# Kernel optimization log

Hardware: AMD Instinct MI355X
Metric: run time of the kernel (lower is better)

The kernel has to match this reference:

```python
import jax, jax.numpy as jnp
import numpy as np

N = 100000
EPS = 1e-5

def gcn_conv(x, W, b, src, dst, n):
    # linear transform first (PyG GCNConv): [N, H]
    h = x @ W
    # add self-loops
    loop = jnp.arange(n, dtype=src.dtype)
    s = jnp.concatenate([src, loop])
    d = jnp.concatenate([dst, loop])
    # symmetric normalization deg^{-1/2}[s] * deg^{-1/2}[d]
    deg = jax.ops.segment_sum(jnp.ones_like(d, dtype=h.dtype), d, num_segments=n)
    dinv = jnp.where(deg > 0, jax.lax.rsqrt(jnp.maximum(deg, 1.0) * 0 + jnp.where(deg > 0, deg, 1.0)), 0.0)
    norm = dinv[s] * dinv[d]
    msg = h[s] * norm[:, None]          # gather + scale: [E+N, H]
    out = jax.ops.segment_sum(msg, d, num_segments=n)  # scatter-add
    return out + b

def batch_norm(x, gamma, beta):
    mu = jnp.mean(x, axis=0)
    var = jnp.mean((x - mu) ** 2, axis=0)  # biased var, as BatchNorm1d training
    return (x - mu) * jax.lax.rsqrt(var + EPS) * gamma + beta

def setup_inputs() -> dict:
    key = jax.random.key(0)
    ks = jax.random.split(key, 8)
    D, H, O = 64, 64, 32
    E = 1600000
    x = jax.random.normal(ks[0], (N, D), dtype=jnp.float32)
    edge_index = jax.random.randint(ks[1], (2, E), 0, N, dtype=jnp.int64)
    W1 = jax.random.normal(ks[2], (D, H), dtype=jnp.float32) / np.sqrt(D)
    b1 = jnp.zeros((H,), dtype=jnp.float32)
    W2 = jax.random.normal(ks[3], (H, H), dtype=jnp.float32) / np.sqrt(H)
    b2 = jnp.zeros((H,), dtype=jnp.float32)
    gamma1 = jnp.ones((H,), dtype=jnp.float32); beta1 = jnp.zeros((H,), dtype=jnp.float32)
    gamma2 = jnp.ones((H,), dtype=jnp.float32); beta2 = jnp.zeros((H,), dtype=jnp.float32)
    Wfc = jax.random.normal(ks[4], (H, O), dtype=jnp.float32) / np.sqrt(H)
    bfc = jnp.zeros((O,), dtype=jnp.float32)
    return {"x": x, "edge_index": edge_index, "W1": W1, "b1": b1, "gamma1": gamma1, "beta1": beta1,
            "W2": W2, "b2": b2, "gamma2": gamma2, "beta2": beta2, "Wfc": Wfc, "bfc": bfc}

def reference(x, edge_index, W1, b1, gamma1, beta1, W2, b2, gamma2, beta2, Wfc, bfc):
    src, dst = edge_index[0], edge_index[1]
    h = jax.nn.relu(gcn_conv(x, W1, b1, src, dst, N))
    h = batch_norm(h, gamma1, beta1)
    h = jax.nn.relu(gcn_conv(h, W2, b2, src, dst, N))
    h = batch_norm(h, gamma2, beta2)
    return h @ Wfc + bfc
```

## Files before the change

kernel.cpp:

```cpp
#include <hip/hip_runtime.h>
#include <hip/hip_bf16.h>
#include <cstdint>
#include <cstddef>

#define NS 8
#define SCHUNK 12500
#define BKB 512
#define SUBC 32

static __device__ __forceinline__ unsigned pack_bf16(float a, float b) {
  __hip_bfloat16 lo = __float2bfloat16(a), hi = __float2bfloat16(b);
  unsigned short ulo = *reinterpret_cast<unsigned short*>(&lo);
  unsigned short uhi = *reinterpret_cast<unsigned short*>(&hi);
  return ((unsigned)uhi << 16) | ulo;
}
static __device__ __forceinline__ float blo(unsigned u) {
  union { unsigned q; float f; } x; x.q = u << 16; return x.f;
}
static __device__ __forceinline__ float bhi(unsigned u) {
  union { unsigned q; float f; } x; x.q = u & 0xffff0000u; return x.f;
}


__launch_bounds__(256)
__global__ void bucket_kernel(const int* __restrict__ src, const int* __restrict__ dst,
                              int E, int cap, unsigned magic,
                              int* __restrict__ bcur,
                              int* __restrict__ bkt_d, int* __restrict__ bkt_s) {
  __shared__ int cnt8[NS], base8[NS], gbase8[NS], cur8[NS];
  __shared__ int stg_d[3200], stg_s[3200];
  int t = threadIdx.x;
  int chunk = (E + BKB - 1) / BKB;
  int ebeg = blockIdx.x * chunk;
  int eend = min(E, ebeg + chunk);
  int nloc = eend - ebeg;
  if (t < NS) { cnt8[t] = 0; cur8[t] = 0; }
  __syncthreads();

  int dl[13], sl[13]; unsigned cl[13];
  int nr = (nloc + 255) >> 8;
#pragma unroll 13
  for (int u = 0; u < nr; ++u) {
    int li = (u << 8) + t;
    bool v = li < nloc;
    int i = ebeg + (v ? li : 0);
    int d = v ? __builtin_nontemporal_load(&dst[i]) : 0;
    int s = v ? __builtin_nontemporal_load(&src[i]) : 0;
    unsigned sli = (unsigned)(((unsigned long long)(unsigned)d * magic) >> 45);
    dl[u] = d; sl[u] = s; cl[u] = sli;
    if (v) atomicAdd(&cnt8[sli], 1);
  }
  __syncthreads();
  if (t == 0) {
    int run = 0;
#pragma unroll
    for (int q = 0; q < NS; ++q) { base8[q] = run; run += cnt8[q]; }
  }
  __syncthreads();
  if (t < NS) gbase8[t] = atomicAdd(&bcur[t], cnt8[t]);
#pragma unroll 13
  for (int u = 0; u < nr; ++u) {
    int li = (u << 8) + t;
    if (li < nloc) {
      unsigned sli = cl[u];
      int pos = atomicAdd(&cur8[sli], 1) + base8[sli];
      stg_d[pos] = dl[u]; stg_s[pos] = sl[u];
    }
  }
  __syncthreads();
#pragma unroll
  for (int q = 0; q < NS; ++q) {
    int c = cnt8[q], b = base8[q], g = gbase8[q];
    int* od = bkt_d + (size_t)q * cap + g;
    int* os = bkt_s + (size_t)q * cap + g;
    for (int i = t; i < c; i += 256) { od[i] = stg_d[b + i]; os[i] = stg_s[b + i]; }
  }
}

__launch_bounds__(1024)
__global__ void count_b_kernel(const int* __restrict__ bkt_d, const int* __restrict__ bcur,
                               int cap, int n, int* __restrict__ partials) {
  __shared__ int hist[SCHUNK];
  int slice = blockIdx.x & (NS - 1), sub = blockIdx.x >> 3;
  int sbase = slice * SCHUNK;
  int bs = bcur[slice];
  const int* bk = bkt_d + (size_t)slice * cap;
  for (int l = threadIdx.x; l < SCHUNK; l += 1024) hist[l] = 0;
  __syncthreads();
  int beg = (int)((long long)sub * bs / SUBC);
  int end = (int)((long long)(sub + 1) * bs / SUBC);
  for (int i = beg + threadIdx.x; i < end; i += 1024)
    atomicAdd(&hist[bk[i] - sbase], 1);
  __syncthreads();
  for (int l = threadIdx.x; l < SCHUNK; l += 1024)
    partials[(size_t)sub * n + sbase + l] = hist[l];
}

__global__ void scan1_kernel(int* __restrict__ partials, int n, int* __restrict__ rowptr,
                             float* __restrict__ dinv, int* __restrict__ bsums) {
  __shared__ int sm[1024];
  int t = threadIdx.x;
  int gid = blockIdx.x * 1024 + t;
  int v = 0;
  if (gid < n) {
#pragma unroll
    for (int s = 0; s < SUBC; ++s) {
      int c = partials[(size_t)s * n + gid];
      partials[(size_t)s * n + gid] = v;
      v += c;
    }
    dinv[gid] = rsqrtf((float)(v + 1));
  }
  sm[t] = v;
  __syncthreads();
  for (int off = 1; off < 1024; off <<= 1) {
    int x = (t >= off) ? sm[t - off] : 0;
    __syncthreads();
    sm[t] += x;
    __syncthreads();
  }
  if (gid < n) rowptr[gid] = sm[t] - v;
  if (t == 1023) bsums[blockIdx.x] = sm[1023];
}

__global__ void scan2_kernel(int* __restrict__ bsums, int nb) {
  __shared__ int sm[1024];
  int t = threadIdx.x;
  int v = (t < nb) ? bsums[t] : 0;
  sm[t] = v;
  __syncthreads();
  for (int off = 1; off < 1024; off <<= 1) {
    int x = (t >= off) ? sm[t - off] : 0;
    __syncthreads();
    sm[t] += x;
    __syncthreads();
  }
  if (t < nb) bsums[t] = sm[t] - v;
}

__global__ void scan3_kernel(int n, int E, int* __restrict__ rowptr, const int* __restrict__ bsums) {
  int i = blockIdx.x * blockDim.x + threadIdx.x;
  if (i < n) rowptr[i] += bsums[i >> 10];
  if (i == 0) rowptr[n] = E;
}

__launch_bounds__(1024)
__global__ void scatter_b_kernel(const int* __restrict__ bkt_d, const int* __restrict__ bkt_s,
                                 const int* __restrict__ bcur, int cap, int n,
                                 const int* __restrict__ rowptr, const int* __restrict__ partials,
                                 int* __restrict__ adj) {
  __shared__ int base[SCHUNK];
  int slice = blockIdx.x & (NS - 1), sub = blockIdx.x >> 3;
  int sbase = slice * SCHUNK;
  int bs = bcur[slice];
  const int* bd = bkt_d + (size_t)slice * cap;
  const int* bsc = bkt_s + (size_t)slice * cap;
  const int* pref = partials + (size_t)sub * n;
  for (int l = threadIdx.x; l < SCHUNK; l += 1024)
    base[l] = rowptr[sbase + l] + pref[sbase + l];
  __syncthreads();
  int beg = (int)((long long)sub * bs / SUBC);
  int end = (int)((long long)(sub + 1) * bs / SUBC);
  for (int i = beg + threadIdx.x; i < end; i += 1024) {
    int d = bd[i], s = bsc[i];
    int pos = atomicAdd(&base[d - sbase], 1);
    adj[pos] = s;
  }
}


template <int OUT, bool BF16OUT, bool BN, bool ABF16>
__launch_bounds__(256)
__global__ void gemm_kernel(const void* __restrict__ Ap, const float* __restrict__ W,
                            const float* __restrict__ bnacc,
                            const float* __restrict__ gamma, const float* __restrict__ beta,
                            const float* __restrict__ bias, const float* __restrict__ rowscale,
                            void* __restrict__ Cout, int n, float invn) {
  constexpr int OQ = OUT / 4;
  __shared__ float lds[64 * 65];
  __shared__ float sc_s[64], sh_s[64];
  int t = threadIdx.x;
  int row0 = blockIdx.x * 64;
  int rows = n - row0; if (rows > 64) rows = 64;

  if (BN) {
    if (t < 64) {
      float su = 0.f, sq = 0.f;
#pragma unroll
      for (int c = 0; c < 8; ++c) {
        su += bnacc[c * 128 + t];
        sq += bnacc[c * 128 + 64 + t];
      }
      float mu = su * invn;
      float var = sq * invn - mu * mu;
      float sc = gamma[t] * rsqrtf(var + 1e-5f);
      sc_s[t] = sc;
      sh_s[t] = fmaf(-mu, sc, beta[t]);
    }
    __syncthreads();
  }

  if (ABF16) {
    const uint4* A4 = (const uint4*)((const unsigned short*)Ap + (size_t)row0 * 64);
#pragma unroll
    for (int j = 0; j < 2; ++j) {
      int idx = t + j * 256;
      int r = idx >> 3, c8 = idx & 7;
      uint4 v = make_uint4(0, 0, 0, 0);
      if (r < rows) v = A4[idx];
      float f[8] = {blo(v.x), bhi(v.x), blo(v.y), bhi(v.y),
                    blo(v.z), bhi(v.z), blo(v.w), bhi(v.w)};
      float* p = &lds[r * 65 + c8 * 8];
#pragma unroll
      for (int q = 0; q < 8; ++q) {
        float xv = f[q];
        if (BN) xv = fmaf(xv, sc_s[c8 * 8 + q], sh_s[c8 * 8 + q]);
        p[q] = xv;
      }
    }
  } else {
    const float4* A4 = (const float4*)((const float*)Ap + (size_t)row0 * 64);
#pragma unroll
    for (int j = 0; j < 4; ++j) {
      int idx = t + j * 256;
      int r = idx >> 4, c4 = idx & 15;
      float4 v = make_float4(0.f, 0.f, 0.f, 0.f);
      if (r < rows) v = A4[idx];
      if (BN) {
        int c = c4 * 4;
        v.x = fmaf(v.x, sc_s[c + 0], sh_s[c + 0]);
        v.y = fmaf(v.y, sc_s[c + 1], sh_s[c + 1]);
        v.z = fmaf(v.z, sc_s[c + 2], sh_s[c + 2]);
        v.w = fmaf(v.w, sc_s[c + 3], sh_s[c + 3]);
      }
      float* p = &lds[r * 65 + c4 * 4];
      p[0] = v.x; p[1] = v.y; p[2] = v.z; p[3] = v.w;
    }
  }
  __syncthreads();

  const int w = __builtin_amdgcn_readfirstlane(t >> 6);
  const int r = t & 63;
  float acc[OQ];
#pragma unroll
  for (int o = 0; o < OQ; ++o) acc[o] = 0.f;
  const float* Ar = &lds[r * 65];
  const float* Wp = W + w * OQ;
  for (int k = 0; k < 64; ++k) {
    float a = Ar[k];
#pragma unroll
    for (int o = 0; o < OQ; ++o) acc[o] = fmaf(a, Wp[k * OUT + o], acc[o]);
  }
  if (rowscale) {
    int rr = row0 + r; if (rr >= n) rr = n - 1;
    float rs = rowscale[rr];
#pragma unroll
    for (int o = 0; o < OQ; ++o) acc[o] *= rs;
  }
  if (bias) {
    const float* Bp = bias + w * OQ;
#pragma unroll
    for (int o = 0; o < OQ; ++o) acc[o] += Bp[o];
  }

  if (r < rows) {
    if (BF16OUT) {
      unsigned pk[OQ / 2];
#pragma unroll
      for (int o2 = 0; o2 < OQ / 2; ++o2) pk[o2] = pack_bf16(acc[2 * o2], acc[2 * o2 + 1]);
      uint4* cp = (uint4*)((__hip_bfloat16*)Cout + (size_t)(row0 + r) * OUT + w * OQ);
#pragma unroll
      for (int j = 0; j < OQ / 8; ++j) {
        uint4 v; v.x = pk[j * 4]; v.y = pk[j * 4 + 1]; v.z = pk[j * 4 + 2]; v.w = pk[j * 4 + 3];
        cp[j] = v;
      }
    } else {
      float4* cp = (float4*)((float*)Cout + (size_t)(row0 + r) * OUT + w * OQ);
#pragma unroll
      for (int j = 0; j < OQ / 4; ++j)
        cp[j] = make_float4(acc[j * 4], acc[j * 4 + 1], acc[j * 4 + 2], acc[j * 4 + 3]);
    }
  }
}


__launch_bounds__(256, 8)
__global__ void agg_kernel(const __hip_bfloat16* __restrict__ g, const int* __restrict__ rowptr,
                           const int* __restrict__ adj, const float* __restrict__ dinv,
                           const float* __restrict__ bias, __hip_bfloat16* __restrict__ out,
                           float* __restrict__ bnacc, int n) {
  const int tid = threadIdx.x;
  const int lane = tid & 63;
  const int wave = tid >> 6;
  const int grp = lane >> 3;
  const int sub = lane & 7;
  const int gw = blockIdx.x * 4 + wave;

  float bias8[8];
  const float4* bp = (const float4*)(bias + sub * 8);
  float4 b0 = bp[0], b1 = bp[1];
  bias8[0]=b0.x; bias8[1]=b0.y; bias8[2]=b0.z; bias8[3]=b0.w;
  bias8[4]=b1.x; bias8[5]=b1.y; bias8[6]=b1.z; bias8[7]=b1.w;

  float s1[8], s2[8];
#pragma unroll
  for (int j = 0; j < 8; ++j) { s1[j] = 0.f; s2[j] = 0.f; }

  const unsigned short* gu = (const unsigned short*)g;

  int d = gw * 8 + grp;
  int beg = rowptr[d];
  int k = rowptr[d + 1] - beg;
  float di = dinv[d];

  const uint4 v0 = *(const uint4*)(gu + (((size_t)d) << 6) + sub * 8);
  float acc[8];
  acc[0] = blo(v0.x); acc[1] = bhi(v0.x);
  acc[2] = blo(v0.y); acc[3] = bhi(v0.y);
  acc[4] = blo(v0.z); acc[5] = bhi(v0.z);
  acc[6] = blo(v0.w); acc[7] = bhi(v0.w);

  int kmax = k;
  kmax = max(kmax, __shfl_xor(kmax, 8));
  kmax = max(kmax, __shfl_xor(kmax, 16));
  kmax = max(kmax, __shfl_xor(kmax, 32));

  for (int j0 = 0; j0 < kmax; j0 += 8) {
#pragma unroll
    for (int u = 0; u < 8; ++u) {
      int idx = j0 + u;
      if (idx < k) {
        int s = adj[beg + idx];
        const uint4 v = *(const uint4*)(gu + (((size_t)s) << 6) + sub * 8);
        acc[0] += blo(v.x); acc[1] += bhi(v.x);
        acc[2] += blo(v.y); acc[3] += bhi(v.y);
        acc[4] += blo(v.z); acc[5] += bhi(v.z);
        acc[6] += blo(v.w); acc[7] += bhi(v.w);
      }
    }
  }

  float o[8];
#pragma unroll
  for (int j = 0; j < 8; ++j) {
    float v = fmaf(acc[j], di, bias8[j]);
    v = fmaxf(v, 0.f);
    o[j] = v;
    s1[j] += v;
    s2[j] = fmaf(v, v, s2[j]);
  }
  uint4 ov;
  ov.x = pack_bf16(o[0], o[1]); ov.y = pack_bf16(o[2], o[3]);
  ov.z = pack_bf16(o[4], o[5]); ov.w = pack_bf16(o[6], o[7]);
  *(uint4*)((unsigned short*)out + (((size_t)d) << 6) + sub * 8) = ov;

#pragma unroll
  for (int j = 0; j < 8; ++j) {
    s1[j] += __shfl_xor(s1[j], 8);  s2[j] += __shfl_xor(s2[j], 8);
    s1[j] += __shfl_xor(s1[j], 16); s2[j] += __shfl_xor(s2[j], 16);
    s1[j] += __shfl_xor(s1[j], 32); s2[j] += __shfl_xor(s2[j], 32);
  }
  __shared__ float redA[4][64], redB[4][64];
  if (lane < 8) {
#pragma unroll
    for (int j = 0; j < 8; ++j) {
      redA[wave][sub * 8 + j] = s1[j];
      redB[wave][sub * 8 + j] = s2[j];
    }
  }
  __syncthreads();
  if (tid < 64) {
    float a = redA[0][tid] + redA[1][tid] + redA[2][tid] + redA[3][tid];
    float b = redB[0][tid] + redB[1][tid] + redB[2][tid] + redB[3][tid];
    float* dst = bnacc + (blockIdx.x & 7) * 128;
    atomicAdd(&dst[tid], a);
    atomicAdd(&dst[64 + tid], b);
  }
}


extern "C" void kernel_launch(void* const* d_in, const int* in_sizes, int n_in,
                              void* d_out, int out_size, void* d_ws, size_t ws_size,
                              hipStream_t stream) {
  const float* x      = (const float*)d_in[0];
  const int*   ei     = (const int*)d_in[1];
  const float* W1     = (const float*)d_in[2];
  const float* b1     = (const float*)d_in[3];
  const float* gamma1 = (const float*)d_in[4];
  const float* beta1  = (const float*)d_in[5];
  const float* W2     = (const float*)d_in[6];
  const float* b2     = (const float*)d_in[7];
  const float* gamma2 = (const float*)d_in[8];
  const float* beta2  = (const float*)d_in[9];
  const float* Wfc    = (const float*)d_in[10];
  const float* bfc    = (const float*)d_in[11];

  int n = in_sizes[0] / 64;
  int E = in_sizes[1] / 2;
  const int* src = ei;
  const int* dst = ei + E;

  char* base = (char*)d_ws;
  size_t off = 0;
  auto alloc = [&](size_t bytes) -> char* {
    char* p = base + off;
    off += (bytes + 255) & ~(size_t)255;
    return p;
  };
  int*   rowptr = (int*)alloc((size_t)(n + 1) * 4);
  int*   adj    = (int*)alloc((size_t)E * 4);
  int*   bsums  = (int*)alloc(1024 * 4);
  float* dinv   = (float*)alloc((size_t)n * 4);
  float* bn     = (float*)alloc(2048 * 4);
  int*   bcur   = (int*)alloc(NS * 4);
  __hip_bfloat16* hbuf = (__hip_bfloat16*)alloc((size_t)n * 64 * 2);
  char*  rraw   = alloc((size_t)n * 64 * 4);
  __hip_bfloat16* rbuf = (__hip_bfloat16*)rraw;
  int cap = 210000;
  int* bkt_d = (int*)rraw;
  int* bkt_s = bkt_d + (size_t)NS * cap;
  int* partials = (int*)hbuf;
  (void)ws_size; (void)n_in; (void)out_size;

  hipMemsetAsync(bn, 0, 2048 * 4, stream);
  hipMemsetAsync(bcur, 0, NS * 4, stream);

  unsigned magic = (unsigned)(((1ULL << 45) + SCHUNK - 1) / SCHUNK);
  bucket_kernel<<<BKB, 256, 0, stream>>>(src, dst, E, cap, magic, bcur, bkt_d, bkt_s);
  count_b_kernel<<<NS * SUBC, 1024, 0, stream>>>(bkt_d, bcur, cap, n, partials);
  int nb = (n + 1023) / 1024;
  scan1_kernel<<<nb, 1024, 0, stream>>>(partials, n, rowptr, dinv, bsums);
  scan2_kernel<<<1, 1024, 0, stream>>>(bsums, nb);
  scan3_kernel<<<(n + 255) / 256, 256, 0, stream>>>(n, E, rowptr, bsums);
  scatter_b_kernel<<<NS * SUBC, 1024, 0, stream>>>(bkt_d, bkt_s, bcur, cap, n,
                                                   rowptr, partials, adj);

  int gg = (n + 63) / 64;
  int ga = n / 32;
  float invn = 1.0f / (float)n;
  gemm_kernel<64, true, false, false><<<gg, 256, 0, stream>>>(
      x, W1, nullptr, nullptr, nullptr, nullptr, dinv, hbuf, n, 0.f);
  agg_kernel<<<ga, 256, 0, stream>>>(hbuf, rowptr, adj, dinv, b1, rbuf, bn, n);
  gemm_kernel<64, true, true, true><<<gg, 256, 0, stream>>>(
      rbuf, W2, bn, gamma1, beta1, nullptr, dinv, hbuf, n, invn);
  agg_kernel<<<ga, 256, 0, stream>>>(hbuf, rowptr, adj, dinv, b2, rbuf, bn + 1024, n);
  gemm_kernel<32, false, true, true><<<gg, 256, 0, stream>>>(
      rbuf, Wfc, bn + 1024, gamma2, beta2, bfc, nullptr, d_out, n, invn);
}
```

Baseline: 289.4 us.

## Split bf16 features into four column slabs and aggregate per slab

The intermediate bf16 feature matrices are stored as four column-major slabs of 16 columns, each N x 16. The GEMM writes and reads that layout, and the aggregation kernel launches four passes, one per slab, with each lane gathering 4 bytes instead of 16. Each slab is 3.2 MB, so the random neighbour gathers of a pass should mostly hit in cache. The kernel also touches a chunk of the slab at block start to warm the cache, and uses nontemporal loads and stores for the adjacency and the output. The cost is that adjacency lists and rowptr are now read four times, and the GEMM's strided slab accesses may coalesce less well.

```diff
diff --git a/kernel.cpp b/kernel.cpp
--- a/kernel.cpp
+++ b/kernel.cpp
@@ -201,13 +201,14 @@
   }
 
   if (ABF16) {
-    const uint4* A4 = (const uint4*)((const unsigned short*)Ap + (size_t)row0 * 64);
+    const uint4* A4 = (const uint4*)Ap;
+    const size_t sstride = (size_t)n * 2;
 #pragma unroll
     for (int j = 0; j < 2; ++j) {
       int idx = t + j * 256;
       int r = idx >> 3, c8 = idx & 7;
       uint4 v = make_uint4(0, 0, 0, 0);
-      if (r < rows) v = A4[idx];
+      if (r < rows) v = A4[(size_t)(c8 >> 1) * sstride + (size_t)(row0 + r) * 2 + (c8 & 1)];
       float f[8] = {blo(v.x), bhi(v.x), blo(v.y), bhi(v.y),
                     blo(v.z), bhi(v.z), blo(v.w), bhi(v.w)};
       float* p = &lds[r * 65 + c8 * 8];
@@ -268,7 +269,7 @@
       unsigned pk[OQ / 2];
 #pragma unroll
       for (int o2 = 0; o2 < OQ / 2; ++o2) pk[o2] = pack_bf16(acc[2 * o2], acc[2 * o2 + 1]);
-      uint4* cp = (uint4*)((__hip_bfloat16*)Cout + (size_t)(row0 + r) * OUT + w * OQ);
+      uint4* cp = (uint4*)((unsigned short*)Cout + (size_t)w * n * 16 + (size_t)(row0 + r) * 16);
 #pragma unroll
       for (int j = 0; j < OQ / 8; ++j) {
         uint4 v; v.x = pk[j * 4]; v.y = pk[j * 4 + 1]; v.z = pk[j * 4 + 2]; v.w = pk[j * 4 + 3];
@@ -288,37 +289,42 @@
 __global__ void agg_kernel(const __hip_bfloat16* __restrict__ g, const int* __restrict__ rowptr,
                            const int* __restrict__ adj, const float* __restrict__ dinv,
                            const float* __restrict__ bias, __hip_bfloat16* __restrict__ out,
-                           float* __restrict__ bnacc, int n) {
+                           float* __restrict__ bnacc, int n, int npb) {
   const int tid = threadIdx.x;
   const int lane = tid & 63;
   const int wave = tid >> 6;
   const int grp = lane >> 3;
   const int sub = lane & 7;
-  const int gw = blockIdx.x * 4 + wave;
-
-  float bias8[8];
-  const float4* bp = (const float4*)(bias + sub * 8);
-  float4 b0 = bp[0], b1 = bp[1];
-  bias8[0]=b0.x; bias8[1]=b0.y; bias8[2]=b0.z; bias8[3]=b0.w;
-  bias8[4]=b1.x; bias8[5]=b1.y; bias8[6]=b1.z; bias8[7]=b1.w;
-
-  float s1[8], s2[8];
-#pragma unroll
-  for (int j = 0; j < 8; ++j) { s1[j] = 0.f; s2[j] = 0.f; }
-
-  const unsigned short* gu = (const unsigned short*)g;
-
-  int d = gw * 8 + grp;
+  const int bi = blockIdx.x;
+  const int pass = bi / npb;
+  const int i = bi - pass * npb;
+  const unsigned short* gs = (const unsigned short*)g + (size_t)pass * n * 16;
+
+  {
+    const uint4* ws = (const uint4*)gs;
+    int cbase = (i >> 3) << 9;
+    int lim = n * 2;
+#pragma unroll
+    for (int u = 0; u < 2; ++u) {
+      int idx = cbase + (u << 8) + tid;
+      if (idx < lim) {
+        uint4 v = ws[idx];
+        asm volatile("" :: "v"(v.x), "v"(v.y), "v"(v.z), "v"(v.w));
+      }
+    }
+  }
+
+  const int d = i * 32 + wave * 8 + grp;
   int beg = rowptr[d];
   int k = rowptr[d + 1] - beg;
   float di = dinv[d];
-
-  const uint4 v0 = *(const uint4*)(gu + (((size_t)d) << 6) + sub * 8);
-  float acc[8];
-  acc[0] = blo(v0.x); acc[1] = bhi(v0.x);
-  acc[2] = blo(v0.y); acc[3] = bhi(v0.y);
-  acc[4] = blo(v0.z); acc[5] = bhi(v0.z);
-  acc[6] = blo(v0.w); acc[7] = bhi(v0.w);
+  const int* ap = adj + beg;
+
+  float b0v = bias[pass * 16 + sub * 2];
+  float b1v = bias[pass * 16 + sub * 2 + 1];
+
+  unsigned v0 = *(const unsigned*)(gs + ((size_t)d << 4) + (sub << 1));
+  float acc0 = blo(v0), acc1 = bhi(v0);
 
   int kmax = k;
   kmax = max(kmax, __shfl_xor(kmax, 8));
@@ -330,51 +336,39 @@
     for (int u = 0; u < 8; ++u) {
       int idx = j0 + u;
       if (idx < k) {
-        int s = adj[beg + idx];
-        const uint4 v = *(const uint4*)(gu + (((size_t)s) << 6) + sub * 8);
-        acc[0] += blo(v.x); acc[1] += bhi(v.x);
-        acc[2] += blo(v.y); acc[3] += bhi(v.y);
-        acc[4] += blo(v.z); acc[5] += bhi(v.z);
-        acc[6] += blo(v.w); acc[7] += bhi(v.w);
-      }
-    }
-  }
-
-  float o[8];
-#pragma unroll
-  for (int j = 0; j < 8; ++j) {
-    float v = fmaf(acc[j], di, bias8[j]);
-    v = fmaxf(v, 0.f);
-    o[j] = v;
-    s1[j] += v;
-    s2[j] = fmaf(v, v, s2[j]);
-  }
-  uint4 ov;
-  ov.x = pack_bf16(o[0], o[1]); ov.y = pack_bf16(o[2], o[3]);
-  ov.z = pack_bf16(o[4], o[5]); ov.w = pack_bf16(o[6], o[7]);
-  *(uint4*)((unsigned short*)out + (((size_t)d) << 6) + sub * 8) = ov;
-
-#pragma unroll
-  for (int j = 0; j < 8; ++j) {
-    s1[j] += __shfl_xor(s1[j], 8);  s2[j] += __shfl_xor(s2[j], 8);
-    s1[j] += __shfl_xor(s1[j], 16); s2[j] += __shfl_xor(s2[j], 16);
-    s1[j] += __shfl_xor(s1[j], 32); s2[j] += __shfl_xor(s2[j], 32);
-  }
-  __shared__ float redA[4][64], redB[4][64];
+        int s = __builtin_nontemporal_load(&ap[idx]);
+        unsigned v = *(const unsigned*)(gs + ((size_t)s << 4) + (sub << 1));
+        acc0 += blo(v); acc1 += bhi(v);
+      }
+    }
+  }
+
+  float o0 = fmaxf(fmaf(acc0, di, b0v), 0.f);
+  float o1 = fmaxf(fmaf(acc1, di, b1v), 0.f);
+  unsigned ov = pack_bf16(o0, o1);
+  __builtin_nontemporal_store(ov,
+      (unsigned*)((unsigned short*)out + (size_t)pass * n * 16 + ((size_t)d << 4) + (sub << 1)));
+
+  float s10 = o0, s11 = o1;
+  float s20 = o0 * o0, s21 = o1 * o1;
+  s10 += __shfl_xor(s10, 8);  s11 += __shfl_xor(s11, 8);
+  s20 += __shfl_xor(s20, 8);  s21 += __shfl_xor(s21, 8);
+  s10 += __shfl_xor(s10, 16); s11 += __shfl_xor(s11, 16);
+  s20 += __shfl_xor(s20, 16); s21 += __shfl_xor(s21, 16);
+  s10 += __shfl_xor(s10, 32); s11 += __shfl_xor(s11, 32);
+  s20 += __shfl_xor(s20, 32); s21 += __shfl_xor(s21, 32);
+  __shared__ float redA[4][16], redB[4][16];
   if (lane < 8) {
-#pragma unroll
-    for (int j = 0; j < 8; ++j) {
-      redA[wave][sub * 8 + j] = s1[j];
-      redB[wave][sub * 8 + j] = s2[j];
-    }
-  }
-  __syncthreads();
-  if (tid < 64) {
+    redA[wave][sub * 2] = s10; redA[wave][sub * 2 + 1] = s11;
+    redB[wave][sub * 2] = s20; redB[wave][sub * 2 + 1] = s21;
+  }
+  __syncthreads();
+  if (tid < 16) {
     float a = redA[0][tid] + redA[1][tid] + redA[2][tid] + redA[3][tid];
     float b = redB[0][tid] + redB[1][tid] + redB[2][tid] + redB[3][tid];
     float* dst = bnacc + (blockIdx.x & 7) * 128;
-    atomicAdd(&dst[tid], a);
-    atomicAdd(&dst[64 + tid], b);
+    atomicAdd(&dst[pass * 16 + tid], a);
+    atomicAdd(&dst[64 + pass * 16 + tid], b);
   }
 }
 
@@ -436,14 +430,15 @@
                                                    rowptr, partials, adj);
 
   int gg = (n + 63) / 64;
-  int ga = n / 32;
+  int npb = n / 32;
+  int ga = 4 * npb;
   float invn = 1.0f / (float)n;
   gemm_kernel<64, true, false, false><<<gg, 256, 0, stream>>>(
       x, W1, nullptr, nullptr, nullptr, nullptr, dinv, hbuf, n, 0.f);
-  agg_kernel<<<ga, 256, 0, stream>>>(hbuf, rowptr, adj, dinv, b1, rbuf, bn, n);
+  agg_kernel<<<ga, 256, 0, stream>>>(hbuf, rowptr, adj, dinv, b1, rbuf, bn, n, npb);
   gemm_kernel<64, true, true, true><<<gg, 256, 0, stream>>>(
       rbuf, W2, bn, gamma1, beta1, nullptr, dinv, hbuf, n, invn);
-  agg_kernel<<<ga, 256, 0, stream>>>(hbuf, rowptr, adj, dinv, b2, rbuf, bn + 1024, n);
+  agg_kernel<<<ga, 256, 0, stream>>>(hbuf, rowptr, adj, dinv, b2, rbuf, bn + 1024, n, npb);
   gemm_kernel<32, false, true, true><<<gg, 256, 0, stream>>>(
       rbuf, Wfc, bn + 1024, gamma2, beta2, bfc, nullptr, d_out, n, invn);
 }
```

New measurement: 474.0 us. 1.64x slower.
